# Optimization experiments

Hardware: AMD Instinct MI355X
Metric: run time of the kernel (lower is better)

The kernel has to match this reference:

```python
import jax, jax.numpy as jnp
import numpy as np
from jax import lax

L = 2        # encoder layers
D = 256      # d_model
H = 8        # nhead
DH = D // H  # head dim
CF = 2       # compression_factor (default in CustomizedAttn)
FF = 2048    # dim_feedforward
B = 10       # batch (forced: null_k has shape (10,1,D))
HH = 40
WW = 40
T = HH * WW  # seq len = 1600
EPS = 1e-5


def setup_inputs() -> dict:
    key = jax.random.key(0)
    ks = jax.random.split(key, 16)
    f = lambda k, shp: jax.random.normal(k, shp, jnp.float32) * 0.02
    return {
        "src": jax.random.normal(ks[0], (B, D, HH, WW), jnp.float32),
        "pos_embed": jax.random.normal(ks[1], (B, D, HH, WW), jnp.float32),
        "Wq": f(ks[2], (L, D, D)),
        "Wk": f(ks[3], (L, D, D)),
        "Wv": f(ks[4], (L, D, D)),
        "Wo": f(ks[5], (L, D, D)),
        "bo": jnp.zeros((L, D), jnp.float32),
        "conv_w": f(ks[6], (L, D, D // H, CF)),  # grouped Conv1d weight [out, in/groups, k]
        "conv_b": jnp.zeros((L, D), jnp.float32),
        "null_k": f(ks[7], (L, B, 1, D)),
        "null_v": f(ks[8], (L, B, 1, D)),
        "ln1_g": jnp.ones((L, D), jnp.float32),
        "ln1_b": jnp.zeros((L, D), jnp.float32),
        "ln2_g": jnp.ones((L, D), jnp.float32),
        "ln2_b": jnp.zeros((L, D), jnp.float32),
        "W1": f(ks[9], (L, FF, D)),
        "b1": jnp.zeros((L, FF), jnp.float32),
        "W2": f(ks[10], (L, D, FF)),
        "b2": jnp.zeros((L, D), jnp.float32),
    }


def _layernorm(x, g, b):
    m = jnp.mean(x, axis=-1, keepdims=True)
    v = jnp.var(x, axis=-1, keepdims=True)
    return (x - m) * lax.rsqrt(v + EPS) * g + b


def _attn(x, pos, Wq, Wk, Wv, Wo, bo, cw, cb, nk, nv):
    # x, pos: [B, T, D]
    qk = x + pos
    q = qk @ Wq.T
    k = qk @ Wk.T
    v = x @ Wv.T
    # torch: padding = cf - t % cf -> always in [1, cf], so padding ALWAYS applied
    pad = CF - (T % CF)
    k = jnp.pad(k, ((0, 0), (pad, 0), (0, 0)))
    v = jnp.pad(v, ((0, 0), (pad, 0), (0, 0)))

    def compress(t_):  # grouped strided Conv1d over time, shared weights for k and v
        y = lax.conv_general_dilated(
            t_.transpose(0, 2, 1), cw, (CF,), "VALID",
            dimension_numbers=("NCH", "OIH", "NCH"), feature_group_count=H)
        return (y + cb[None, :, None]).transpose(0, 2, 1)

    k = jnp.concatenate([nk, compress(k)], axis=1)  # [B, Tc+10, D]
    v = jnp.concatenate([nv, compress(v)], axis=1)
    split = lambda t_: t_.reshape(B, t_.shape[1], H, DH).transpose(0, 2, 1, 3)
    qh, kh, vh = split(q), split(k), split(v)
    # NOTE: scale uses FULL d_model (d ** -0.5), faithful to the source.
    dots = jnp.einsum("bhid,bhjd->bhij", qh, kh) * (D ** -0.5)
    # NOTE: the source computes softmax(dots) but then overwrites it with
    # dropout(dots); at inference attention weights are the raw scaled dots.
    out = jnp.einsum("bhij,bhjd->bhid", dots, vh)
    out = out.transpose(0, 2, 1, 3).reshape(B, T, D)
    return out @ Wo.T + bo


def reference(src, pos_embed, Wq, Wk, Wv, Wo, bo, conv_w, conv_b, null_k, null_v,
              ln1_g, ln1_b, ln2_g, ln2_b, W1, b1, W2, b2):
    x = src.reshape(B, D, T).transpose(0, 2, 1)        # [B, T, D]
    pos = pos_embed.reshape(B, D, T).transpose(0, 2, 1)
    for l in range(L):
        a = _attn(x, pos, Wq[l], Wk[l], Wv[l], Wo[l], bo[l],
                  conv_w[l], conv_b[l], null_k[l], null_v[l])
        x = _layernorm(x + a, ln1_g[l], ln1_b[l])
        ff = jnp.maximum(x @ W1[l].T + b1[l], 0.0) @ W2[l].T + b2[l]
        x = _layernorm(x + ff, ln2_g[l], ln2_b[l])
    return x.transpose(0, 2, 1).reshape(B, D, HH, WW)
```

## Files before the change

kernel.cpp:

```cpp
#include <hip/hip_runtime.h>
#include <math.h>

typedef __attribute__((ext_vector_type(8))) short short8;
typedef __attribute__((ext_vector_type(4))) short short4v;
typedef __attribute__((ext_vector_type(4))) float f32x4;
typedef unsigned int u32;

constexpr int Bsz = 10;
constexpr int Dm  = 256;
constexpr int Hh  = 8;
constexpr int Tt  = 1600;
constexpr int FFd = 2048;
constexpr int Tkv = 802;
constexpr int JCH = 8;
constexpr size_t Fsz  = (size_t)Bsz * Tt * Dm;
constexpr size_t PAD  = 65536;
constexpr size_t KVsz = (size_t)Bsz * Tkv * Dm;
constexpr size_t FHsz = (size_t)Bsz * Tt * FFd;
constexpr size_t WBsz = 2621440;

__device__ float g_x[Fsz];
__device__ float g_qk[Fsz];
__device__ float g_t[Fsz];
__device__ float g_kc[KVsz];
__device__ float g_vc[KVsz];
__device__ float g_kvm[(size_t)Bsz * Hh * 32 * 32];
__device__ float g_kvp[(size_t)JCH * Bsz * Hh * 32 * 32];
__device__ float g_pos[Fsz];
__device__ unsigned short g_xb[Fsz + PAD];
__device__ unsigned short g_qkb[Fsz + PAD];
__device__ unsigned short g_tb[Fsz + PAD];
__device__ unsigned short g_qb[Fsz + PAD];
__device__ unsigned short g_ffh[FHsz + PAD];
__device__ unsigned short g_wb[WBsz];
__device__ unsigned short g_wo2[(size_t)Bsz * Dm * Dm];

__device__ __forceinline__ float* selbuf(int id) {
  switch (id) {
    case 0: return g_x;
    case 1: return g_qk;
    case 2: return g_t;
    case 3: return g_kc;
    case 4: return g_vc;
    default: return g_kvm;
  }
}
__device__ __forceinline__ unsigned short* selbufb(int id) {
  switch (id) {
    case 0: return g_xb;
    case 1: return g_qkb;
    case 2: return g_tb;
    case 3: return g_ffh;
    default: return g_qb;
  }
}

__device__ __forceinline__ unsigned short f2b(float x) {
  unsigned int u = __float_as_uint(x);
  u += 0x7FFFu + ((u >> 16) & 1u);
  return (unsigned short)(u >> 16);
}
__device__ __forceinline__ float b2f(unsigned short u) {
  return __uint_as_float(((unsigned int)u) << 16);
}

__global__ __launch_bounds__(256) void wconv_all_k(
    const float* __restrict__ Wk, const float* __restrict__ Wq,
    const float* __restrict__ Wv, const float* __restrict__ Wo,
    const float* __restrict__ W1, const float* __restrict__ W2) {
  const int i = blockIdx.x * 256 + threadIdx.x;
  float v;
  if (i < 262144) {
    const int l = i >> 17, r = i & 131071;
    v = (r < 65536) ? Wk[l * 65536 + r] : Wq[l * 65536 + (r - 65536)];
  } else if (i < 393216) {
    v = Wv[i - 262144];
  } else if (i < 524288) {
    v = Wo[i - 393216];
  } else if (i < 1572864) {
    v = W1[i - 524288];
  } else {
    v = W2[i - 1572864];
  }
  g_wb[i] = f2b(v);
}

__global__ __launch_bounds__(256) void trans_in2_k(const float* __restrict__ src,
                                                   const float* __restrict__ pose) {
  __shared__ float ts[32][33];
  __shared__ float tp[32][33];
  const int tx = threadIdx.x & 31, ty = threadIdx.x >> 5;
  const int t0 = blockIdx.x * 32, d0 = blockIdx.y * 32, b = blockIdx.z;
  #pragma unroll
  for (int i = ty; i < 32; i += 8) {
    const size_t gi = ((size_t)(b * Dm + d0 + i)) * Tt + t0 + tx;
    ts[i][tx] = src[gi];
    tp[i][tx] = pose[gi];
  }
  __syncthreads();
  #pragma unroll
  for (int i = ty; i < 32; i += 8) {
    const size_t idx = ((size_t)(b * Tt + t0 + i)) * Dm + d0 + tx;
    const float s = ts[tx][i], p = tp[tx][i];
    g_x[idx] = s;
    g_pos[idx] = p;
    g_xb[idx] = f2b(s);
    g_qkb[idx] = f2b(s + p);
  }
}

__global__ __launch_bounds__(256) void trans_out_k(float* out) {
  __shared__ float tile[32][33];
  const int tx = threadIdx.x & 31, ty = threadIdx.x >> 5;
  const int t0 = blockIdx.x * 32, d0 = blockIdx.y * 32, b = blockIdx.z;
  #pragma unroll
  for (int i = ty; i < 32; i += 8)
    tile[i][tx] = g_x[((size_t)(b * Tt + t0 + i)) * Dm + d0 + tx];
  __syncthreads();
  #pragma unroll
  for (int i = ty; i < 32; i += 8)
    out[((size_t)(b * Dm + d0 + i)) * Tt + t0 + tx] = tile[tx][i];
}

template<int BN, bool DUAL, bool PERB, bool RELU, bool BIAS, bool CBF16>
__global__ __launch_bounds__(256) void gemm2_k(
    int Aid, int woff, const float* __restrict__ bias, int Cid, int C2id,
    int NB, int M, int N, int K) {
  constexpr int BM = 128, BK = 64;
  constexpr int ACH = BM * 8;
  constexpr int BCH = BN * 8;
  constexpr int NW = BN / 32;
  __shared__ short8 As8[3][ACH];
  __shared__ short8 Bs8[3][BCH];
  const int tid = threadIdx.x;
  const int lane = tid & 63, wid = tid >> 6;
  const int wr = wid >> 1, wc = wid & 1;

  const int nwg = gridDim.x;
  const int bid = blockIdx.x;
  const int q = nwg >> 3, r = nwg & 7;
  const int xcd = bid & 7, seq = bid >> 3;
  const int wgid = (xcd < r ? xcd * (q + 1) : r * (q + 1) + (xcd - r) * q) + seq;

  int m0, n0, mlim;
  const unsigned short* W16;
  if constexpr (PERB) {
    const int per = 13 * NB;
    const int b = wgid / per;
    const int rem = wgid - b * per;
    m0 = b * Tt + (rem / NB) * BM;
    n0 = (rem % NB) * BN;
    mlim = b * Tt + Tt;
    W16 = g_wo2 + (size_t)b * 65536;
  } else {
    m0 = (wgid / NB) * BM;
    n0 = (wgid % NB) * BN;
    mlim = M;
    W16 = g_wb + woff;
  }

  const unsigned short* A16 = selbufb(Aid);
  const bool second = DUAL && (n0 >= 256);
  float* Cf = selbuf(second ? C2id : Cid);
  unsigned short* C16 = selbufb(second ? C2id : Cid);
  const int gn0 = second ? n0 - 256 : n0;
  const int cstride = DUAL ? 256 : N;

  f32x4 acc[4][NW];
  #pragma unroll
  for (int m = 0; m < 4; ++m)
    #pragma unroll
    for (int n = 0; n < NW; ++n) acc[m][n] = (f32x4){0.f, 0.f, 0.f, 0.f};

  const int lkc = lane >> 4, lrc = lane & 15;

  auto stage = [&](int t, int buf) {
    const int k0 = t * BK;
    #pragma unroll
    for (int i = 0; i < ACH / 256; ++i) {
      const int c = tid + i * 256;
      const int row = c >> 3, kc = c & 7;
      const unsigned short* gs = A16 + (size_t)(m0 + row) * K + k0 +
                                 ((kc ^ (row & 7)) << 3);
      __builtin_amdgcn_global_load_lds(
          (const __attribute__((address_space(1))) u32*)gs,
          (__attribute__((address_space(3))) u32*)&As8[buf][c], 16, 0, 0);
    }
    #pragma unroll
    for (int i = 0; i < BCH / 256; ++i) {
      const int c = tid + i * 256;
      const int row = c >> 3, kc = c & 7;
      const unsigned short* gs = W16 + (size_t)(n0 + row) * K + k0 +
                                 ((kc ^ (row & 7)) << 3);
      __builtin_amdgcn_global_load_lds(
          (const __attribute__((address_space(1))) u32*)gs,
          (__attribute__((address_space(3))) u32*)&Bs8[buf][c], 16, 0, 0);
    }
  };

  const int nt = K / BK;
  stage(0, 0);
  if (nt > 1) stage(1, 1);
  int cur = 0, nxt = 2;
  for (int t = 0; t < nt; ++t) {
    if (t + 1 < nt) {
      if constexpr (BN == 64)
        asm volatile("s_waitcnt vmcnt(6)" ::: "memory");
      else
        asm volatile("s_waitcnt vmcnt(8)" ::: "memory");
    } else {
      asm volatile("s_waitcnt vmcnt(0)" ::: "memory");
    }
    __builtin_amdgcn_sched_barrier(0);
    __builtin_amdgcn_s_barrier();
    __builtin_amdgcn_sched_barrier(0);
    if (t + 2 < nt) stage(t + 2, nxt);
    #pragma unroll
    for (int kk = 0; kk < 2; ++kk) {
      short8 af[4], bf[NW];
      #pragma unroll
      for (int m = 0; m < 4; ++m) {
        const int r2 = wr * 64 + m * 16 + lrc;
        af[m] = As8[cur][r2 * 8 + ((kk * 4 + lkc) ^ (r2 & 7))];
      }
      #pragma unroll
      for (int n = 0; n < NW; ++n) {
        const int cn = wc * (BN / 2) + n * 16 + lrc;
        bf[n] = Bs8[cur][cn * 8 + ((kk * 4 + lkc) ^ (cn & 7))];
      }
      #pragma unroll
      for (int m = 0; m < 4; ++m)
        #pragma unroll
        for (int n = 0; n < NW; ++n)
          acc[m][n] = __builtin_amdgcn_mfma_f32_16x16x32_bf16(
              af[m], bf[n], acc[m][n], 0, 0, 0);
    }
    cur = (cur == 2) ? 0 : cur + 1;
    nxt = (nxt == 2) ? 0 : nxt + 1;
  }

  constexpr int CSTR = (BN == 64) ? BN + 4 : BN;
  float* ldsC = (float*)&As8[0][0];
  {
    asm volatile("s_waitcnt vmcnt(0)" ::: "memory");
    __builtin_amdgcn_s_barrier();
    const int r0 = lkc * 4;
    #pragma unroll
    for (int m = 0; m < 4; ++m)
      #pragma unroll
      for (int n = 0; n < NW; ++n) {
        const int col = wc * (BN / 2) + n * 16 + lrc;
        #pragma unroll
        for (int j = 0; j < 4; ++j)
          ldsC[(wr * 64 + m * 16 + r0 + j) * CSTR + col] = acc[m][n][j];
      }
    __syncthreads();
  }
  if constexpr (CBF16) {
    constexpr int CH = BM * BN / 8;
    #pragma unroll
    for (int i = 0; i < CH / 256; ++i) {
      const int c = tid + i * 256;
      const int rowl = c / (BN / 8), col8 = (c % (BN / 8)) * 8;
      if (PERB && m0 + rowl >= mlim) continue;
      short8 v;
      #pragma unroll
      for (int j = 0; j < 8; ++j) {
        float x = ldsC[rowl * CSTR + col8 + j];
        if (BIAS) x += bias[gn0 + col8 + j];
        if (RELU) x = fmaxf(x, 0.f);
        v[j] = (short)f2b(x);
      }
      *(short8*)(C16 + (size_t)(m0 + rowl) * cstride + gn0 + col8) = v;
    }
  } else {
    constexpr int CH = BM * BN / 4;
    #pragma unroll
    for (int i = 0; i < CH / 256; ++i) {
      const int c = tid + i * 256;
      const int rowl = c / (BN / 4), col4 = (c % (BN / 4)) * 4;
      if (PERB && m0 + rowl >= mlim) continue;
      float4 v;
      float* pv = &v.x;
      #pragma unroll
      for (int j = 0; j < 4; ++j) {
        float x = ldsC[rowl * CSTR + col4 + j];
        if (BIAS) x += bias[gn0 + col4 + j];
        if (RELU) x = fmaxf(x, 0.f);
        pv[j] = x;
      }
      *(float4*)(Cf + (size_t)(m0 + rowl) * cstride + gn0 + col4) = v;
    }
  }
}

__global__ __launch_bounds__(256) void compress2_k(
    const float* __restrict__ cw, const float* __restrict__ cb,
    const float* __restrict__ nk, const float* __restrict__ nv) {
  __shared__ float rows[32][256];
  const int tc0 = 1 + blockIdx.x * 16;
  const int b = blockIdx.y;
  const int z = blockIdx.z;
  const int tid = threadIdx.x;
  const int o = tid;
  const int g = o >> 5;

  const unsigned short* srcbuf = z ? g_ffh : g_tb;
  const float* nul = z ? nv : nk;
  float* outb = (z ? g_vc : g_kc) + (size_t)b * Tkv * Dm;

  const int r0g = 2 * tc0 - 2;
  const unsigned short* src = srcbuf + ((size_t)b * Tt + r0g) * Dm;
  #pragma unroll
  for (int i = 0; i < 4; ++i) {
    const int c = tid + i * 256;
    const int row = c >> 5, off = (c & 31) * 8;
    short8 v = *(const short8*)(src + (size_t)row * 256 + off);
    #pragma unroll
    for (int j = 0; j < 8; ++j)
      rows[row][off + j] = b2f((unsigned short)v[j]);
  }

  float we[32], wo[32];
  {
    const float4* wp = (const float4*)(cw + o * 64);
    #pragma unroll
    for (int i = 0; i < 16; ++i) {
      float4 w4 = wp[i];
      we[i * 2 + 0] = w4.x; wo[i * 2 + 0] = w4.y;
      we[i * 2 + 1] = w4.z; wo[i * 2 + 1] = w4.w;
    }
  }
  const float bias = cb[o];
  if (blockIdx.x == 0) {
    outb[o] = nul[b * Dm + o];
    outb[Dm + o] = bias;
  }
  __syncthreads();

  float* outp = outb + o;
  #pragma unroll
  for (int t = 0; t < 16; ++t) {
    const int lr = 2 * t;
    const float* p0 = &rows[lr][g * 32];
    const float* p1 = &rows[lr + 1][g * 32];
    float acc = bias;
    #pragma unroll
    for (int i4 = 0; i4 < 8; ++i4) {
      float4 a0 = *(const float4*)(p0 + i4 * 4);
      float4 a1 = *(const float4*)(p1 + i4 * 4);
      acc = fmaf(we[i4 * 4 + 0], a0.x, acc);
      acc = fmaf(we[i4 * 4 + 1], a0.y, acc);
      acc = fmaf(we[i4 * 4 + 2], a0.z, acc);
      acc = fmaf(we[i4 * 4 + 3], a0.w, acc);
      acc = fmaf(wo[i4 * 4 + 0], a1.x, acc);
      acc = fmaf(wo[i4 * 4 + 1], a1.y, acc);
      acc = fmaf(wo[i4 * 4 + 2], a1.z, acc);
      acc = fmaf(wo[i4 * 4 + 3], a1.w, acc);
    }
    outp[(size_t)(1 + tc0 + t) * Dm] = acc;
  }
}

__global__ __launch_bounds__(256) void kvout1_k() {
  __shared__ float kl[8][32];
  __shared__ float vl[8][32];
  const int bh = blockIdx.x;
  const int js = blockIdx.y;
  const int b = bh >> 3, h = bh & 7;
  const int j0 = js * 101;
  const int jend = (j0 + 101 < Tkv) ? j0 + 101 : Tkv;

  const int tid = threadIdx.x;
  const int lr = tid >> 5;
  const int lc = tid & 31;
  const int e = tid >> 3;
  const int d0 = (tid & 7) * 4;

  float a0 = 0.f, a1 = 0.f, a2 = 0.f, a3 = 0.f;
  const size_t base = (size_t)b * Tkv * Dm + h * 32;

  for (int jc = j0; jc < jend; jc += 8) {
    const int jr = jc + lr;
    if (jr < jend) {
      kl[lr][lc] = g_kc[base + (size_t)jr * Dm + lc];
      vl[lr][lc] = g_vc[base + (size_t)jr * Dm + lc];
    } else {
      kl[lr][lc] = 0.f;
      vl[lr][lc] = 0.f;
    }
    __syncthreads();
    #pragma unroll
    for (int r = 0; r < 8; ++r) {
      const float kf = kl[r][e];
      const float* vr = &vl[r][d0];
      a0 = fmaf(kf, vr[0], a0);
      a1 = fmaf(kf, vr[1], a1);
      a2 = fmaf(kf, vr[2], a2);
      a3 = fmaf(kf, vr[3], a3);
    }
    __syncthreads();
  }
  float* op = g_kvp + ((size_t)js * 80 + bh) * 1024 + e * 32 + d0;
  op[0] = a0; op[1] = a1; op[2] = a2; op[3] = a3;
}

__global__ __launch_bounds__(256) void kvout2_k() {
  const int bh = blockIdx.x;
  const int tid = threadIdx.x;
  const int e = tid >> 3;
  const int d0 = (tid & 7) * 4;
  float a0 = 0.f, a1 = 0.f, a2 = 0.f, a3 = 0.f;
  #pragma unroll
  for (int s = 0; s < JCH; ++s) {
    const float* p = g_kvp + ((size_t)s * 80 + bh) * 1024 + e * 32 + d0;
    a0 += p[0]; a1 += p[1]; a2 += p[2]; a3 += p[3];
  }
  float* op = g_kvm + (size_t)bh * 1024 + e * 32 + d0;
  op[0] = a0 * 0.0625f;
  op[1] = a1 * 0.0625f;
  op[2] = a2 * 0.0625f;
  op[3] = a3 * 0.0625f;
}

__global__ __launch_bounds__(256) void wo2_k(int wooff) {
  const int n = blockIdx.x, b = blockIdx.y;
  const int he = threadIdx.x;
  const int h = he >> 5, e = he & 31;
  const float* kp = g_kvm + ((size_t)(b * Hh + h) * 32 + e) * 32;
  const unsigned short* wp = g_wb + wooff + (size_t)n * Dm + h * 32;
  float acc = 0.f;
  #pragma unroll
  for (int d = 0; d < 32; ++d) acc = fmaf(kp[d], b2f(wp[d]), acc);
  g_wo2[(size_t)b * 65536 + (size_t)n * Dm + he] = f2b(acc);
}

__global__ __launch_bounds__(256) void ln_k(int did, int did2, const float* g,
                                            const float* beta, int do_pos) {
  const int lane = threadIdx.x & 63;
  const int wave = threadIdx.x >> 6;
  const size_t row = (size_t)blockIdx.x * 4 + wave;
  float4 xv = ((const float4*)g_x)[row * 64 + lane];
  float4 dv = ((const float4*)selbuf(did))[row * 64 + lane];
  float v[4] = {xv.x + dv.x, xv.y + dv.y, xv.z + dv.z, xv.w + dv.w};
  if (did2 >= 0) {
    float4 d2 = ((const float4*)selbuf(did2))[row * 64 + lane];
    v[0] += d2.x; v[1] += d2.y; v[2] += d2.z; v[3] += d2.w;
  }
  float sum = v[0] + v[1] + v[2] + v[3];
  float sq = v[0]*v[0] + v[1]*v[1] + v[2]*v[2] + v[3]*v[3];
  #pragma unroll
  for (int off = 32; off; off >>= 1) {
    sum += __shfl_xor(sum, off);
    sq  += __shfl_xor(sq, off);
  }
  const float mean = sum * (1.f / 256.f);
  const float var = sq * (1.f / 256.f) - mean * mean;
  const float rs = rsqrtf(var + 1e-5f);
  float4 gg = ((const float4*)g)[lane];
  float4 bb = ((const float4*)beta)[lane];
  float4 ov;
  ov.x = (v[0] - mean) * rs * gg.x + bb.x;
  ov.y = (v[1] - mean) * rs * gg.y + bb.y;
  ov.z = (v[2] - mean) * rs * gg.z + bb.z;
  ov.w = (v[3] - mean) * rs * gg.w + bb.w;
  ((float4*)g_x)[row * 64 + lane] = ov;
  short4v sv;
  sv[0] = (short)f2b(ov.x); sv[1] = (short)f2b(ov.y);
  sv[2] = (short)f2b(ov.z); sv[3] = (short)f2b(ov.w);
  *(short4v*)&g_xb[(row * 64 + lane) * 4] = sv;
  if (do_pos) {
    float4 pv = ((const float4*)g_pos)[row * 64 + lane];
    short4v qv;
    qv[0] = (short)f2b(ov.x + pv.x); qv[1] = (short)f2b(ov.y + pv.y);
    qv[2] = (short)f2b(ov.z + pv.z); qv[3] = (short)f2b(ov.w + pv.w);
    *(short4v*)&g_qkb[(row * 64 + lane) * 4] = qv;
  }
}

extern "C" void kernel_launch(void* const* d_in, const int* in_sizes, int n_in,
                              void* d_out, int out_size, void* d_ws, size_t ws_size,
                              hipStream_t stream) {
  const float* src  = (const float*)d_in[0];
  const float* pose = (const float*)d_in[1];
  const float* Wq   = (const float*)d_in[2];
  const float* Wk   = (const float*)d_in[3];
  const float* Wv   = (const float*)d_in[4];
  const float* Wo   = (const float*)d_in[5];
  const float* bo   = (const float*)d_in[6];
  const float* cw   = (const float*)d_in[7];
  const float* cb   = (const float*)d_in[8];
  const float* nk   = (const float*)d_in[9];
  const float* nv   = (const float*)d_in[10];
  const float* ln1g = (const float*)d_in[11];
  const float* ln1b = (const float*)d_in[12];
  const float* ln2g = (const float*)d_in[13];
  const float* ln2b = (const float*)d_in[14];
  const float* W1   = (const float*)d_in[15];
  const float* b1   = (const float*)d_in[16];
  const float* W2   = (const float*)d_in[17];
  const float* b2   = (const float*)d_in[18];

  const int MT = Bsz * Tt;
  const dim3 tgrid(Tt / 32, Dm / 32, Bsz);

  const int OV = 262144, OO = 393216, O1 = 524288, O2 = 1572864;
  wconv_all_k<<<10240, 256, 0, stream>>>(Wk, Wq, Wv, Wo, W1, W2);
  trans_in2_k<<<tgrid, 256, 0, stream>>>(src, pose);

  const int MB = MT / 128;
  for (int l = 0; l < 2; ++l) {
    const float* bo_l = bo + (size_t)l * Dm;
    const float* cw_l = cw + (size_t)l * Dm * 64;
    const float* cb_l = cb + (size_t)l * Dm;
    const float* nk_l = nk + (size_t)l * Bsz * Dm;
    const float* nv_l = nv + (size_t)l * Bsz * Dm;
    const float* b1_l = b1 + (size_t)l * FFd;
    const float* b2_l = b2 + (size_t)l * Dm;
    const int wkq = l * 131072;
    const int wv = OV + l * 65536, wo = OO + l * 65536;
    const int w1 = O1 + l * 524288, w2 = O2 + l * 524288;

    gemm2_k<64, true, false, false, false, true><<<8 * MB, 256, 0, stream>>>(
        1, wkq, nullptr, 2, 4, 8, MT, 512, Dm);
    gemm2_k<64, false, false, false, false, true><<<4 * MB, 256, 0, stream>>>(
        0, wv, nullptr, 3, 3, 4, MT, Dm, Dm);
    compress2_k<<<dim3(50, Bsz, 2), 256, 0, stream>>>(cw_l, cb_l, nk_l, nv_l);
    kvout1_k<<<dim3(Bsz * Hh, JCH), 256, 0, stream>>>();
    kvout2_k<<<Bsz * Hh, 256, 0, stream>>>();
    wo2_k<<<dim3(Dm, Bsz), 256, 0, stream>>>(wo);
    gemm2_k<64, false, true, false, true, false><<<Bsz * 13 * 4, 256, 0, stream>>>(
        4, 0, bo_l, 2, 2, 4, MT, Dm, Dm);
    ln_k<<<MT / 4, 256, 0, stream>>>(2, -1, ln1g + l * Dm, ln1b + l * Dm, 0);

    gemm2_k<64, false, false, true, true, true><<<32 * MB, 256, 0, stream>>>(
        0, w1, b1_l, 3, 3, 32, MT, FFd, Dm);
    gemm2_k<64, false, false, false, true, false><<<4 * MB, 256, 0, stream>>>(
        3, w2, b2_l, 1, 1, 4, MT, Dm, FFd);
    ln_k<<<MT / 4, 256, 0, stream>>>(1, -1, ln2g + l * Dm, ln2b + l * Dm,
                                     l == 0 ? 1 : 0);
  }

  trans_out_k<<<tgrid, 256, 0, stream>>>((float*)d_out);
}
```

Measured before the change: 368.6 us.

## Add specialized K=256 GEMM kernel with 128x128 tiles and 512 threads

Introduces gemmr_k, a GEMM specialized for K=256 that uses 128x128 tiles, 8 waves, and two half-K stages with no multi-buffering. It stores results straight from registers instead of going through LDS, and raises wave priority around the MFMA loop. It replaces the generic 64-wide-tile kernel for the QK, V, Wo and W1 projections, while W2 keeps the old kernel. The intent is more data reuse per tile and fewer workgroups, but load and compute no longer overlap within a block, and the stores are now scalar and less coalesced.

Result: slower. 385.4 us (+4.5%).

```diff
diff --git a/kernel.cpp b/kernel.cpp
--- a/kernel.cpp
+++ b/kernel.cpp
@@ -122,20 +122,16 @@
     out[((size_t)(b * Dm + d0 + i)) * Tt + t0 + tx] = tile[tx][i];
 }
 
-template<int BN, bool DUAL, bool PERB, bool RELU, bool BIAS, bool CBF16>
-__global__ __launch_bounds__(256) void gemm2_k(
+template<bool DUAL, bool PERB, bool RELU, bool BIAS, bool CBF16>
+__global__ __launch_bounds__(512, 4) void gemmr_k(
     int Aid, int woff, const float* __restrict__ bias, int Cid, int C2id,
-    int NB, int M, int N, int K) {
-  constexpr int BM = 128, BK = 64;
-  constexpr int ACH = BM * 8;
-  constexpr int BCH = BN * 8;
-  constexpr int NW = BN / 32;
-  __shared__ short8 As8[3][ACH];
-  __shared__ short8 Bs8[3][BCH];
+    int NB, int N) {
+  constexpr int BM = 128, BN = 128, K = 256, KH = 128;
+  __shared__ short8 As8[BM * 16];
+  __shared__ short8 Bs8[BN * 16];
   const int tid = threadIdx.x;
   const int lane = tid & 63, wid = tid >> 6;
-  const int wr = wid >> 1, wc = wid & 1;
-
+  const int wr = wid >> 2, wc = wid & 3;
   const int nwg = gridDim.x;
   const int bid = blockIdx.x;
   const int q = nwg >> 3, r = nwg & 7;
@@ -155,7 +151,7 @@
   } else {
     m0 = (wgid / NB) * BM;
     n0 = (wgid % NB) * BN;
-    mlim = M;
+    mlim = 1 << 30;
     W16 = g_wb + woff;
   }
 
@@ -164,7 +160,113 @@
   float* Cf = selbuf(second ? C2id : Cid);
   unsigned short* C16 = selbufb(second ? C2id : Cid);
   const int gn0 = second ? n0 - 256 : n0;
-  const int cstride = DUAL ? 256 : N;
+  const int cst = DUAL ? 256 : N;
+  const int lkc = lane >> 4, lrc = lane & 15;
+
+  f32x4 acc[4][2];
+  #pragma unroll
+  for (int m = 0; m < 4; ++m)
+    #pragma unroll
+    for (int n = 0; n < 2; ++n) acc[m][n] = (f32x4){0.f, 0.f, 0.f, 0.f};
+
+  #pragma unroll
+  for (int h = 0; h < 2; ++h) {
+    const int k0 = h * KH;
+    if (h) __builtin_amdgcn_s_barrier();
+    #pragma unroll
+    for (int i = 0; i < (BM * 16) / 512; ++i) {
+      const int c = tid + i * 512;
+      const int row = c >> 4, kc = c & 15;
+      const unsigned short* gs = A16 + (size_t)(m0 + row) * K + k0 +
+                                 ((kc ^ (row & 15)) << 3);
+      __builtin_amdgcn_global_load_lds(
+          (const __attribute__((address_space(1))) u32*)gs,
+          (__attribute__((address_space(3))) u32*)&As8[c], 16, 0, 0);
+    }
+    #pragma unroll
+    for (int i = 0; i < (BN * 16) / 512; ++i) {
+      const int c = tid + i * 512;
+      const int row = c >> 4, kc = c & 15;
+      const unsigned short* gs = W16 + (size_t)(n0 + row) * K + k0 +
+                                 ((kc ^ (row & 15)) << 3);
+      __builtin_amdgcn_global_load_lds(
+          (const __attribute__((address_space(1))) u32*)gs,
+          (__attribute__((address_space(3))) u32*)&Bs8[c], 16, 0, 0);
+    }
+    asm volatile("s_waitcnt vmcnt(0)" ::: "memory");
+    __builtin_amdgcn_sched_barrier(0);
+    __builtin_amdgcn_s_barrier();
+
+    __builtin_amdgcn_s_setprio(1);
+    #pragma unroll
+    for (int s = 0; s < 4; ++s) {
+      short8 af[4], bf[2];
+      #pragma unroll
+      for (int m = 0; m < 4; ++m) {
+        const int r2 = wr * 64 + m * 16 + lrc;
+        af[m] = As8[r2 * 16 + ((s * 4 + lkc) ^ (r2 & 15))];
+      }
+      #pragma unroll
+      for (int n = 0; n < 2; ++n) {
+        const int cn = wc * 32 + n * 16 + lrc;
+        bf[n] = Bs8[cn * 16 + ((s * 4 + lkc) ^ (cn & 15))];
+      }
+      #pragma unroll
+      for (int m = 0; m < 4; ++m)
+        #pragma unroll
+        for (int n = 0; n < 2; ++n)
+          acc[m][n] = __builtin_amdgcn_mfma_f32_16x16x32_bf16(
+              af[m], bf[n], acc[m][n], 0, 0, 0);
+    }
+    __builtin_amdgcn_s_setprio(0);
+  }
+
+  const int r0 = lkc * 4;
+  #pragma unroll
+  for (int m = 0; m < 4; ++m) {
+    const int gmb = m0 + wr * 64 + m * 16 + r0;
+    #pragma unroll
+    for (int n = 0; n < 2; ++n) {
+      const int gn = gn0 + wc * 32 + n * 16 + lrc;
+      const float bb = BIAS ? bias[gn] : 0.f;
+      #pragma unroll
+      for (int j = 0; j < 4; ++j) {
+        if constexpr (PERB) { if (gmb + j >= mlim) continue; }
+        float v = acc[m][n][j] + bb;
+        if (RELU) v = fmaxf(v, 0.f);
+        if (CBF16) C16[(size_t)(gmb + j) * cst + gn] = f2b(v);
+        else       Cf[(size_t)(gmb + j) * cst + gn] = v;
+      }
+    }
+  }
+}
+
+template<int BN, bool RELU, bool BIAS, bool CBF16>
+__global__ __launch_bounds__(256) void gemm2_k(
+    int Aid, int woff, const float* __restrict__ bias, int Cid,
+    int NB, int M, int N, int K) {
+  constexpr int BM = 128, BK = 64;
+  constexpr int ACH = BM * 8;
+  constexpr int BCH = BN * 8;
+  constexpr int NW = BN / 32;
+  __shared__ short8 As8[3][ACH];
+  __shared__ short8 Bs8[3][BCH];
+  const int tid = threadIdx.x;
+  const int lane = tid & 63, wid = tid >> 6;
+  const int wr = wid >> 1, wc = wid & 1;
+
+  const int nwg = gridDim.x;
+  const int bid = blockIdx.x;
+  const int q = nwg >> 3, r = nwg & 7;
+  const int xcd = bid & 7, seq = bid >> 3;
+  const int wgid = (xcd < r ? xcd * (q + 1) : r * (q + 1) + (xcd - r) * q) + seq;
+
+  const int m0 = (wgid / NB) * BM;
+  const int n0 = (wgid % NB) * BN;
+  const unsigned short* W16 = g_wb + woff;
+  const unsigned short* A16 = selbufb(Aid);
+  float* Cf = selbuf(Cid);
+  unsigned short* C16 = selbufb(Cid);
 
   f32x4 acc[4][NW];
   #pragma unroll
@@ -204,10 +306,7 @@
   int cur = 0, nxt = 2;
   for (int t = 0; t < nt; ++t) {
     if (t + 1 < nt) {
-      if constexpr (BN == 64)
-        asm volatile("s_waitcnt vmcnt(6)" ::: "memory");
-      else
-        asm volatile("s_waitcnt vmcnt(8)" ::: "memory");
+      asm volatile("s_waitcnt vmcnt(6)" ::: "memory");
     } else {
       asm volatile("s_waitcnt vmcnt(0)" ::: "memory");
     }
@@ -262,16 +361,15 @@
     for (int i = 0; i < CH / 256; ++i) {
       const int c = tid + i * 256;
       const int rowl = c / (BN / 8), col8 = (c % (BN / 8)) * 8;
-      if (PERB && m0 + rowl >= mlim) continue;
       short8 v;
       #pragma unroll
       for (int j = 0; j < 8; ++j) {
         float x = ldsC[rowl * CSTR + col8 + j];
-        if (BIAS) x += bias[gn0 + col8 + j];
+        if (BIAS) x += bias[n0 + col8 + j];
         if (RELU) x = fmaxf(x, 0.f);
         v[j] = (short)f2b(x);
       }
-      *(short8*)(C16 + (size_t)(m0 + rowl) * cstride + gn0 + col8) = v;
+      *(short8*)(C16 + (size_t)(m0 + rowl) * N + n0 + col8) = v;
     }
   } else {
     constexpr int CH = BM * BN / 4;
@@ -279,17 +377,16 @@
     for (int i = 0; i < CH / 256; ++i) {
       const int c = tid + i * 256;
       const int rowl = c / (BN / 4), col4 = (c % (BN / 4)) * 4;
-      if (PERB && m0 + rowl >= mlim) continue;
       float4 v;
       float* pv = &v.x;
       #pragma unroll
       for (int j = 0; j < 4; ++j) {
         float x = ldsC[rowl * CSTR + col4 + j];
-        if (BIAS) x += bias[gn0 + col4 + j];
+        if (BIAS) x += bias[n0 + col4 + j];
         if (RELU) x = fmaxf(x, 0.f);
         pv[j] = x;
       }
-      *(float4*)(Cf + (size_t)(m0 + rowl) * cstride + gn0 + col4) = v;
+      *(float4*)(Cf + (size_t)(m0 + rowl) * N + n0 + col4) = v;
     }
   }
 }
@@ -521,22 +618,22 @@
     const int wv = OV + l * 65536, wo = OO + l * 65536;
     const int w1 = O1 + l * 524288, w2 = O2 + l * 524288;
 
-    gemm2_k<64, true, false, false, false, true><<<8 * MB, 256, 0, stream>>>(
-        1, wkq, nullptr, 2, 4, 8, MT, 512, Dm);
-    gemm2_k<64, false, false, false, false, true><<<4 * MB, 256, 0, stream>>>(
-        0, wv, nullptr, 3, 3, 4, MT, Dm, Dm);
+    gemmr_k<true, false, false, false, true><<<4 * MB, 512, 0, stream>>>(
+        1, wkq, nullptr, 2, 4, 4, 512);
+    gemmr_k<false, false, false, false, true><<<2 * MB, 512, 0, stream>>>(
+        0, wv, nullptr, 3, 3, 2, 256);
     compress2_k<<<dim3(50, Bsz, 2), 256, 0, stream>>>(cw_l, cb_l, nk_l, nv_l);
     kvout1_k<<<dim3(Bsz * Hh, JCH), 256, 0, stream>>>();
     kvout2_k<<<Bsz * Hh, 256, 0, stream>>>();
     wo2_k<<<dim3(Dm, Bsz), 256, 0, stream>>>(wo);
-    gemm2_k<64, false, true, false, true, false><<<Bsz * 13 * 4, 256, 0, stream>>>(
-        4, 0, bo_l, 2, 2, 4, MT, Dm, Dm);
+    gemmr_k<false, true, false, true, false><<<Bsz * 13 * 2, 512, 0, stream>>>(
+        4, 0, bo_l, 2, 2, 2, 256);
     ln_k<<<MT / 4, 256, 0, stream>>>(2, -1, ln1g + l * Dm, ln1b + l * Dm, 0);
 
-    gemm2_k<64, false, false, true, true, true><<<32 * MB, 256, 0, stream>>>(
-        0, w1, b1_l, 3, 3, 32, MT, FFd, Dm);
-    gemm2_k<64, false, false, false, true, false><<<4 * MB, 256, 0, stream>>>(
-        3, w2, b2_l, 1, 1, 4, MT, Dm, FFd);
+    gemmr_k<false, false, true, true, true><<<16 * MB, 512, 0, stream>>>(
+        0, w1, b1_l, 3, 3, 16, FFd);
+    gemm2_k<64, false, true, false><<<4 * MB, 256, 0, stream>>>(
+        3, w2, b2_l, 1, 4, MT, Dm, FFd);
     ln_k<<<MT / 4, 256, 0, stream>>>(1, -1, ln2g + l * Dm, ln2b + l * Dm,
                                      l == 0 ? 1 : 0);
   }
```

## Fuse FFN up-projection, ReLU and down-projection into one kernel with split-K halves

Applied to the files above, without the earlier changes.

Replaces the two FFN GEMM launches with a single fused kernel. Each block keeps a 128-row activation tile in LDS, computes hidden chunks of 32 columns with bias and ReLU into LDS as bf16, and immediately accumulates them into the down-projection. The FF dimension is split in two halves across blocks that write partial sums to separate buffers, which the LayerNorm kernel then adds. The large hidden activation no longer makes a round trip through global memory. In exchange only 250 blocks of 512 threads run, each with small per-chunk MFMA work and frequent barriers. The GEMM wait count is also simplified to a single vmcnt value.

Result: slower. 378.7 us (+2.7%).

```diff
diff --git a/kernel.cpp b/kernel.cpp
--- a/kernel.cpp
+++ b/kernel.cpp
@@ -204,10 +204,7 @@
   int cur = 0, nxt = 2;
   for (int t = 0; t < nt; ++t) {
     if (t + 1 < nt) {
-      if constexpr (BN == 64)
-        asm volatile("s_waitcnt vmcnt(6)" ::: "memory");
-      else
-        asm volatile("s_waitcnt vmcnt(8)" ::: "memory");
+      asm volatile("s_waitcnt vmcnt(6)" ::: "memory");
     } else {
       asm volatile("s_waitcnt vmcnt(0)" ::: "memory");
     }
@@ -290,6 +287,162 @@
         pv[j] = x;
       }
       *(float4*)(Cf + (size_t)(m0 + rowl) * cstride + gn0 + col4) = v;
+    }
+  }
+}
+
+__global__ __launch_bounds__(512, 1) void gemmf_k(
+    int Aid, int w1off, int w2off, const float* __restrict__ b1p,
+    const float* __restrict__ b2p) {
+  constexpr int BM = 128, NCH = 32;
+  __shared__ short8 Al[BM * 32];
+  __shared__ short8 w1c[2][1024];
+  __shared__ short8 w2c[2][1024];
+  __shared__ short8 h8[BM * 4];
+  __shared__ float b1f[1024];
+  const int tid = threadIdx.x;
+  const int lane = tid & 63, wid = tid >> 6;
+  const int lkc = lane >> 4, lrc = lane & 15;
+  const int nwg = gridDim.x, bid = blockIdx.x;
+  const int q = nwg >> 3, r = nwg & 7;
+  const int xcd = bid & 7, seq = bid >> 3;
+  const int wgid = (xcd < r ? xcd * (q + 1) : r * (q + 1) + (xcd - r) * q) + seq;
+  const int half = (wgid >= 125) ? 1 : 0;
+  const int m0 = (wgid - half * 125) * BM;
+  const int hb = half * 1024;
+  const unsigned short* A16 = selbufb(Aid);
+  const unsigned short* W1p = g_wb + w1off;
+  const unsigned short* W2p = g_wb + w2off;
+  float* Cf = half ? g_t : g_qk;
+
+  #pragma unroll
+  for (int i = 0; i < 8; ++i) {
+    const int c = tid + i * 512;
+    const int row = c >> 5, kc = c & 31;
+    const unsigned short* gs = A16 + (size_t)(m0 + row) * 256 +
+                               ((kc ^ (row & 31)) << 3);
+    __builtin_amdgcn_global_load_lds(
+        (const __attribute__((address_space(1))) u32*)gs,
+        (__attribute__((address_space(3))) u32*)&Al[c], 16, 0, 0);
+  }
+  #pragma unroll
+  for (int i = 0; i < 2; ++i) {
+    const int c = tid + i * 512;
+    __builtin_amdgcn_global_load_lds(
+        (const __attribute__((address_space(1))) u32*)(b1p + hb + c),
+        (__attribute__((address_space(3))) u32*)&b1f[c], 4, 0, 0);
+  }
+  auto stage_w = [&](int ch, int buf) {
+    const int kb = hb + ch * 32;
+    #pragma unroll
+    for (int i = 0; i < 2; ++i) {
+      const int c = tid + i * 512;
+      const int row = c >> 5, kc = c & 31;
+      const unsigned short* gs = W1p + (size_t)(kb + row) * 256 +
+                                 ((kc ^ (row & 31)) << 3);
+      __builtin_amdgcn_global_load_lds(
+          (const __attribute__((address_space(1))) u32*)gs,
+          (__attribute__((address_space(3))) u32*)&w1c[buf][c], 16, 0, 0);
+    }
+    #pragma unroll
+    for (int i = 0; i < 2; ++i) {
+      const int c = tid + i * 512;
+      const int row = c >> 2, kc = c & 3;
+      const int g = (kc ^ (row & 3) ^ ((row >> 2) & 3)) & 3;
+      const unsigned short* gs = W2p + (size_t)row * 2048 + kb + (g << 3);
+      __builtin_amdgcn_global_load_lds(
+          (const __attribute__((address_space(1))) u32*)gs,
+          (__attribute__((address_space(3))) u32*)&w2c[buf][c], 16, 0, 0);
+    }
+  };
+  stage_w(0, 0);
+
+  const int wr = wid >> 2, wc = wid & 3;
+  f32x4 acc2[4][4];
+  #pragma unroll
+  for (int m = 0; m < 4; ++m)
+    #pragma unroll
+    for (int n = 0; n < 4; ++n) acc2[m][n] = (f32x4){0.f, 0.f, 0.f, 0.f};
+
+  for (int ch = 0; ch < NCH; ++ch) {
+    const int cur = ch & 1;
+    if (ch) {
+      __builtin_amdgcn_sched_barrier(0);
+      __builtin_amdgcn_s_barrier();
+      __builtin_amdgcn_sched_barrier(0);
+    }
+    if (ch + 1 < NCH) {
+      stage_w(ch + 1, cur ^ 1);
+      asm volatile("s_waitcnt vmcnt(4)" ::: "memory");
+    } else {
+      asm volatile("s_waitcnt vmcnt(0)" ::: "memory");
+    }
+    __builtin_amdgcn_sched_barrier(0);
+    __builtin_amdgcn_s_barrier();
+    __builtin_amdgcn_sched_barrier(0);
+
+    f32x4 a1[2];
+    a1[0] = (f32x4){0.f, 0.f, 0.f, 0.f};
+    a1[1] = (f32x4){0.f, 0.f, 0.f, 0.f};
+    const int r1 = wid * 16 + lrc;
+    #pragma unroll
+    for (int s = 0; s < 8; ++s) {
+      short8 af = Al[r1 * 32 + ((s * 4 + lkc) ^ (r1 & 31))];
+      #pragma unroll
+      for (int n = 0; n < 2; ++n) {
+        const int cn = n * 16 + lrc;
+        short8 bf = w1c[cur][cn * 32 + ((s * 4 + lkc) ^ (cn & 31))];
+        a1[n] = __builtin_amdgcn_mfma_f32_16x16x32_bf16(af, bf, a1[n], 0, 0, 0);
+      }
+    }
+    unsigned short* h16 = (unsigned short*)h8;
+    #pragma unroll
+    for (int n = 0; n < 2; ++n) {
+      const int col = n * 16 + lrc;
+      const float bb = b1f[ch * 32 + col];
+      #pragma unroll
+      for (int j = 0; j < 4; ++j) {
+        const int row = wid * 16 + lkc * 4 + j;
+        float v = fmaxf(a1[n][j] + bb, 0.f);
+        const int g = ((col >> 3) ^ (row & 3) ^ ((row >> 2) & 3)) & 3;
+        h16[row * 32 + g * 8 + (col & 7)] = f2b(v);
+      }
+    }
+    asm volatile("s_waitcnt lgkmcnt(0)" ::: "memory");
+    __builtin_amdgcn_sched_barrier(0);
+    __builtin_amdgcn_s_barrier();
+    __builtin_amdgcn_sched_barrier(0);
+
+    short8 af2[4], bf2[4];
+    #pragma unroll
+    for (int m = 0; m < 4; ++m) {
+      const int r2 = wr * 64 + m * 16 + lrc;
+      af2[m] = h8[r2 * 4 + ((lkc ^ (r2 & 3) ^ ((r2 >> 2) & 3)) & 3)];
+    }
+    #pragma unroll
+    for (int n = 0; n < 4; ++n) {
+      const int cn = wc * 64 + n * 16 + lrc;
+      bf2[n] = w2c[cur][cn * 4 + ((lkc ^ (cn & 3) ^ ((cn >> 2) & 3)) & 3)];
+    }
+    #pragma unroll
+    for (int m = 0; m < 4; ++m)
+      #pragma unroll
+      for (int n = 0; n < 4; ++n)
+        acc2[m][n] = __builtin_amdgcn_mfma_f32_16x16x32_bf16(
+            af2[m], bf2[n], acc2[m][n], 0, 0, 0);
+  }
+
+  const int r0 = lkc * 4;
+  #pragma unroll
+  for (int m = 0; m < 4; ++m) {
+    const int gm = m0 + wr * 64 + m * 16 + r0;
+    #pragma unroll
+    for (int n = 0; n < 4; ++n) {
+      const int gn = wc * 64 + n * 16 + lrc;
+      const float bb = (half == 0) ? b2p[gn] : 0.f;
+      #pragma unroll
+      for (int j = 0; j < 4; ++j)
+        Cf[(size_t)(gm + j) * 256 + gn] = acc2[m][n][j] + bb;
     }
   }
 }
@@ -533,11 +686,8 @@
         4, 0, bo_l, 2, 2, 4, MT, Dm, Dm);
     ln_k<<<MT / 4, 256, 0, stream>>>(2, -1, ln1g + l * Dm, ln1b + l * Dm, 0);
 
-    gemm2_k<64, false, false, true, true, true><<<32 * MB, 256, 0, stream>>>(
-        0, w1, b1_l, 3, 3, 32, MT, FFd, Dm);
-    gemm2_k<64, false, false, false, true, false><<<4 * MB, 256, 0, stream>>>(
-        3, w2, b2_l, 1, 1, 4, MT, Dm, FFd);
-    ln_k<<<MT / 4, 256, 0, stream>>>(1, -1, ln2g + l * Dm, ln2b + l * Dm,
+    gemmf_k<<<250, 512, 0, stream>>>(0, w1, w2, b1_l, b2_l);
+    ln_k<<<MT / 4, 256, 0, stream>>>(1, 2, ln2g + l * Dm, ln2b + l * Dm,
                                      l == 0 ? 1 : 0);
   }
 
```
